# Kernel optimization log

Measured on AMD Instinct MI355X. Metric: run time of the kernel, lower is better.

The kernel has to match this reference:

```python
import math
import jax, jax.numpy as jnp
import numpy as np

B, L, D_MODEL, N_HEADS = 4, 4096, 1024, 16
HEAD_DIM = D_MODEL // N_HEADS
NUM_LANDMARKS = 128


def setup_inputs() -> dict:
    key = jax.random.key(0)
    ks = jax.random.split(key, 7)
    s = 1.0 / math.sqrt(D_MODEL)
    return {
        "x": jax.random.normal(ks[0], (B, L, D_MODEL), dtype=jnp.float32),
        "Wq": jax.random.uniform(ks[1], (D_MODEL, D_MODEL), jnp.float32, -s, s),
        "bq": jax.random.uniform(ks[2], (D_MODEL,), jnp.float32, -s, s),
        "Wk": jax.random.uniform(ks[3], (D_MODEL, D_MODEL), jnp.float32, -s, s),
        "bk": jax.random.uniform(ks[4], (D_MODEL,), jnp.float32, -s, s),
        "Wv": jax.random.uniform(ks[5], (D_MODEL, D_MODEL), jnp.float32, -s, s),
        "bv": jax.random.uniform(ks[6], (D_MODEL,), jnp.float32, -s, s),
    }


def _split_heads(t):
    b, l, _ = t.shape
    return t.reshape(b, l, N_HEADS, HEAD_DIM).transpose(0, 2, 1, 3)  # [b,h,l,d]


def _iterative_inv(mat, n_iter=6):
    # Newton-Schulz pseudo-inverse on [b,h,m,m]; 'original' init uses global max.
    I = jnp.eye(mat.shape[-1], dtype=mat.dtype)
    K = mat
    V = K.swapaxes(-1, -2) / jnp.max(jnp.sum(K, axis=-2))
    for _ in range(n_iter):
        KV = jnp.matmul(K, V)
        V = jnp.matmul(0.25 * V, 13.0 * I - jnp.matmul(KV, 15.0 * I - jnp.matmul(KV, 7.0 * I - KV)))
    return V


def reference(x, Wq, bq, Wk, bk, Wv, bv):
    Q = _split_heads(x @ Wq.T + bq)
    K = _split_heads(x @ Wk.T + bk)
    V = _split_heads(x @ Wv.T + bv)
    b, h, l, d = Q.shape
    # mask is internally all-ones (module overwrites any passed mask), so the
    # -1e9*(1-mask) bias term is identically zero and mask-multiplies are no-ops.
    scale = 1.0 / math.sqrt(math.sqrt(HEAD_DIM))
    Q = Q * scale
    K = K * scale
    seg = l // NUM_LANDMARKS
    Q_lm = Q.reshape(b, h, NUM_LANDMARKS, seg, d).mean(axis=-2)  # [b,h,m,d]
    K_lm = K.reshape(b, h, NUM_LANDMARKS, seg, d).mean(axis=-2)
    kernel_1 = jax.nn.softmax(jnp.einsum('bhld,bhmd->bhlm', Q, K_lm), axis=-1)   # [b,h,l,m]
    kernel_2 = jax.nn.softmax(jnp.einsum('bhmd,bhnd->bhmn', Q_lm, K_lm), axis=-1)  # [b,h,m,m]
    kernel_3 = jax.nn.softmax(jnp.einsum('bhmd,bhld->bhml', Q_lm, K), axis=-1)   # [b,h,m,l]
    X = jnp.matmul(jnp.matmul(kernel_1, _iterative_inv(kernel_2)), jnp.matmul(kernel_3, V))  # [b,h,l,d]
    out = X.transpose(0, 2, 1, 3).reshape(b, l, h * d)
    return out
```

## Files before the change

kernel.cpp:

```cpp
#include <hip/hip_runtime.h>
#include <hip/hip_bf16.h>
#include <stdint.h>

#define DEV __device__ __forceinline__

typedef __attribute__((ext_vector_type(8))) short bf16x8;
typedef __attribute__((ext_vector_type(4))) short short4v;
typedef __attribute__((ext_vector_type(4))) float f32x4;

static constexpr int LL = 4096;
static constexpr int NH = 16;
static constexpr int HD = 64;
static constexpr int DM = 1024;
static constexpr int NL = 128;
static constexpr int BH = 64;
static constexpr int NSPLIT = 8;
static constexpr float QK_SCALE = 0.35355339059327379f;

DEV short f2bf(float f) {
  union { __hip_bfloat16 h; short s; } u;
  u.h = __float2bfloat16(f);
  return u.s;
}
DEV float bf2f(unsigned short s) {
  union { unsigned u; float f; } u;
  u.u = ((unsigned)s) << 16;
  return u.f;
}
DEV float clampf(float v) {
  return fminf(fmaxf(v, -1e6f), 1e6f);
}

DEV f32x4 mfma16(bf16x8 a, bf16x8 b, f32x4 c) {
  return __builtin_amdgcn_mfma_f32_16x16x32_bf16(a, b, c, 0, 0, 0);
}

DEV void gl2lds16(const void* g, void* l) {
  __builtin_amdgcn_global_load_lds(
      (const __attribute__((address_space(1))) void*)g,
      (__attribute__((address_space(3))) void*)l, 16, 0, 0);
}

DEV void split1(float f, short& hi, short& lo) {
  unsigned u = __float_as_uint(f);
  hi = (short)(u >> 16);
  lo = f2bf(f - __uint_as_float(u & 0xffff0000u));
}

DEV void split8(const float* av, bf16x8& hv, bf16x8& lv) {
#pragma unroll
  for (int e = 0; e < 8; e++) {
    short hi, lo;
    split1(av[e], hi, lo);
    hv[e] = hi;
    lv[e] = lo;
  }
}

__global__ __launch_bounds__(256) void probe_kernel(
    const unsigned short* p0, const unsigned short* p1, const unsigned short* p2,
    const unsigned short* p3, const unsigned short* p4, const unsigned short* p5,
    const unsigned short* p6, int* flags)
{
  const unsigned short* ps[7] = {p0, p1, p2, p3, p4, p5, p6};
  const unsigned short* p = ps[blockIdx.x];
  const int t = threadIdx.x;
  __shared__ int cnt;
  if (t == 0) cnt = 0;
  __syncthreads();
  int c = 0;
  for (int i = t; i < 512; i += 256) {
    unsigned e = (p[2 * i] >> 7) & 0xFF;
    if (e > 90 && e < 160) c++;
  }
  atomicAdd(&cnt, c);
  __syncthreads();
  if (t == 0) flags[blockIdx.x] = (cnt < 358) ? 1 : 0;
}

__global__ __launch_bounds__(256) void cvtx_kernel(
    const void* __restrict__ src, const int* __restrict__ flags, int fidx,
    unsigned short* __restrict__ dst, int n8)
{
  const int f32 = flags[fidx];
  for (int i = blockIdx.x * 256 + threadIdx.x; i < n8; i += gridDim.x * 256) {
    if (f32) {
      const float* s = (const float*)src + (size_t)i * 8;
      f32x4 a = *(const f32x4*)s;
      f32x4 b = *(const f32x4*)(s + 4);
      bf16x8 o;
      o[0] = f2bf(a[0]); o[1] = f2bf(a[1]); o[2] = f2bf(a[2]); o[3] = f2bf(a[3]);
      o[4] = f2bf(b[0]); o[5] = f2bf(b[1]); o[6] = f2bf(b[2]); o[7] = f2bf(b[3]);
      *(bf16x8*)(dst + (size_t)i * 8) = o;
    } else {
      *(bf16x8*)(dst + (size_t)i * 8) =
          *(const bf16x8*)((const unsigned short*)src + (size_t)i * 8);
    }
  }
}

__global__ __launch_bounds__(256) void cvtw_kernel(
    const void* __restrict__ Wq, const void* __restrict__ Wk, const void* __restrict__ Wv,
    const void* __restrict__ bq, const void* __restrict__ bk, const void* __restrict__ bv,
    const int* __restrict__ flags,
    unsigned short* __restrict__ Wb, float* __restrict__ bb)
{
  const int bid = blockIdx.x, t = threadIdx.x;
  if (bid < 1536) {
    const int q = bid / 512;
    const int i = (bid % 512) * 256 + t;
    const void* src = (q == 0) ? Wq : ((q == 1) ? Wk : Wv);
    unsigned short* dst = Wb + (size_t)q * DM * DM;
    if (flags[1 + 2 * q]) {
      const float* s = (const float*)src + (size_t)i * 8;
      f32x4 a = *(const f32x4*)s;
      f32x4 b = *(const f32x4*)(s + 4);
      bf16x8 o;
      o[0] = f2bf(a[0]); o[1] = f2bf(a[1]); o[2] = f2bf(a[2]); o[3] = f2bf(a[3]);
      o[4] = f2bf(b[0]); o[5] = f2bf(b[1]); o[6] = f2bf(b[2]); o[7] = f2bf(b[3]);
      *(bf16x8*)(dst + (size_t)i * 8) = o;
    } else {
      *(bf16x8*)(dst + (size_t)i * 8) =
          *(const bf16x8*)((const unsigned short*)src + (size_t)i * 8);
    }
  } else {
    for (int i = t; i < 3 * DM; i += 256) {
      int q = i >> 10, idx = i & 1023;
      const void* src = (q == 0) ? bq : ((q == 1) ? bk : bv);
      bb[i] = flags[2 + 2 * q] ? ((const float*)src)[idx]
                               : bf2f(((const unsigned short*)src)[idx]);
    }
  }
}

__global__ __launch_bounds__(256, 2) void proj_kernel(
    const unsigned short* __restrict__ xb,
    const unsigned short* __restrict__ Wb,
    const float* __restrict__ bb,
    unsigned short* __restrict__ Qo, unsigned short* __restrict__ Ko,
    unsigned short* __restrict__ Vo,
    float* __restrict__ Qlm, float* __restrict__ Klm)
{
  __shared__ __align__(16) short As[2][128 * 32];
  __shared__ __align__(16) short Bs[2][128 * 32];

  const int t = threadIdx.x;
  const int w = t >> 6;
  const int l = t & 63;
  const int lane16 = l & 15, lgrp = l >> 4;

  const int bid = blockIdx.x;
  const int mt = bid & 127;
  const int nt = bid >> 7;
  const int which = nt >> 3;
  const int m0 = mt * 128;
  const int ncol0 = (nt & 7) * 128;

  unsigned short* outp = (which == 0) ? Qo : ((which == 1) ? Ko : Vo);
  const float scl = (which == 2) ? 1.0f : QK_SCALE;

  const int srow = w * 16 + (l >> 2);
  const int skc = (l & 3) * 8;
  const unsigned short* gA = xb + (size_t)(m0 + srow) * DM + skc;
  const unsigned short* gB = Wb + (size_t)which * DM * DM + (size_t)(ncol0 + srow) * DM + skc;
  short* lA0 = As[0] + w * 512;
  short* lA1 = As[1] + w * 512;
  short* lB0 = Bs[0] + w * 512;
  short* lB1 = Bs[1] + w * 512;

  const int wm = (w >> 1) * 64;
  const int wn = (w & 1) * 64;

  f32x4 acc[4][4];
#pragma unroll
  for (int i = 0; i < 4; i++)
#pragma unroll
    for (int j = 0; j < 4; j++) acc[i][j] = f32x4{0.f, 0.f, 0.f, 0.f};

  for (int kk = 0; kk < DM; kk += 64) {
    gl2lds16(gA + kk, lA0);
    gl2lds16(gA + kk + 64 * DM, lA0 + 2048);
    gl2lds16(gA + kk + 32, lA1);
    gl2lds16(gA + kk + 32 + 64 * DM, lA1 + 2048);
    gl2lds16(gB + kk, lB0);
    gl2lds16(gB + kk + 64 * DM, lB0 + 2048);
    gl2lds16(gB + kk + 32, lB1);
    gl2lds16(gB + kk + 32 + 64 * DM, lB1 + 2048);
    __syncthreads();
#pragma unroll
    for (int kc = 0; kc < 2; kc++) {
      bf16x8 af[4], bfv[4];
#pragma unroll
      for (int i = 0; i < 4; i++) {
        af[i]  = *(const bf16x8*)&As[kc][(wm + i * 16 + lane16) * 32 + lgrp * 8];
        bfv[i] = *(const bf16x8*)&Bs[kc][(wn + i * 16 + lane16) * 32 + lgrp * 8];
      }
#pragma unroll
      for (int i = 0; i < 4; i++)
#pragma unroll
        for (int j = 0; j < 4; j++)
          acc[i][j] = mfma16(af[i], bfv[j], acc[i][j]);
    }
    __syncthreads();
  }

  const int b = m0 >> 12;
  const int hh = (ncol0 + wn) >> 6;
  float bv4[4];
#pragma unroll
  for (int j = 0; j < 4; j++)
    bv4[j] = bb[which * DM + ncol0 + wn + j * 16 + lane16];

  float seg[2][4];
#pragma unroll
  for (int s = 0; s < 2; s++)
#pragma unroll
    for (int j = 0; j < 4; j++) seg[s][j] = 0.f;

#pragma unroll
  for (int i = 0; i < 4; i++) {
#pragma unroll
    for (int j = 0; j < 4; j++) {
#pragma unroll
      for (int r = 0; r < 4; r++) {
        float v = (acc[i][j][r] + bv4[j]) * scl;
        int row = wm + i * 16 + lgrp * 4 + r;
        int li = (m0 + row) & 4095;
        int dd = (wn + j * 16 + lane16) & 63;
        outp[(((size_t)(b * NH + hh)) * LL + li) * HD + dd] = (unsigned short)f2bf(v);
        seg[i >> 1][j] += v;
      }
    }
  }
  if (which < 2) {
    float* lmb = (which == 0) ? Qlm : Klm;
#pragma unroll
    for (int s = 0; s < 2; s++) {
#pragma unroll
      for (int j = 0; j < 4; j++) {
        float ssum = seg[s][j];
        ssum += __shfl_xor(ssum, 16, 64);
        ssum += __shfl_xor(ssum, 32, 64);
        if (lgrp == 0) {
          int m = ((m0 + wm + s * 32) & 4095) >> 5;
          int dd = (wn + j * 16 + lane16) & 63;
          lmb[(((size_t)(b * NH + hh)) * NL + m) * HD + dd] = clampf(ssum * (1.0f / 32.0f));
        }
      }
    }
  }
}

__global__ void lmcvt_kernel(const float* __restrict__ qf, const float* __restrict__ kf,
                             unsigned short* __restrict__ qb, unsigned short* __restrict__ kb)
{
  int i = blockIdx.x * 256 + threadIdx.x;
  if (i < BH * NL * HD) {
    qb[i] = (unsigned short)f2bf(qf[i]);
    kb[i] = (unsigned short)f2bf(kf[i]);
  }
}

__global__ __launch_bounds__(256, 1) void k2_kernel(
    const float* __restrict__ Qlm, const float* __restrict__ Klm,
    float* __restrict__ k2, float* __restrict__ colsum_g)
{
  __shared__ float cs[NL];
  const int bid = blockIdx.x;
  const int bh = bid >> 3;
  const int rc = bid & 7;
  const int t = threadIdx.x;
  const int r = t >> 4;
  const int c = t & 15;
  const int row = rc * 16 + r;
  const float* Q = Qlm + ((size_t)bh * NL + row) * HD;
  const float* K = Klm + (size_t)bh * NL * HD;
  float* k2p = k2 + (size_t)bh * NL * NL;

  for (int i = t; i < NL; i += 256) cs[i] = 0.f;

  f32x4 q4[16];
#pragma unroll
  for (int d = 0; d < 16; d++) q4[d] = *(const f32x4*)&Q[d * 4];

  float dots[8];
#pragma unroll
  for (int g = 0; g < 8; g++) {
    const float* kr = K + (size_t)(c + g * 16) * HD;
    float s = 0.f;
#pragma unroll
    for (int d = 0; d < 16; d++) {
      f32x4 k4 = *(const f32x4*)&kr[d * 4];
      s += q4[d][0] * k4[0];
      s += q4[d][1] * k4[1];
      s += q4[d][2] * k4[2];
      s += q4[d][3] * k4[3];
    }
    dots[g] = s;
  }

  float mx = dots[0];
#pragma unroll
  for (int g = 1; g < 8; g++) mx = fmaxf(mx, dots[g]);
  mx = fmaxf(mx, __shfl_xor(mx, 1, 16));
  mx = fmaxf(mx, __shfl_xor(mx, 2, 16));
  mx = fmaxf(mx, __shfl_xor(mx, 4, 16));
  mx = fmaxf(mx, __shfl_xor(mx, 8, 16));

  float sum = 0.f;
#pragma unroll
  for (int g = 0; g < 8; g++) {
    float e = __expf(dots[g] - mx);
    dots[g] = e;
    sum += e;
  }
  sum += __shfl_xor(sum, 1, 16);
  sum += __shfl_xor(sum, 2, 16);
  sum += __shfl_xor(sum, 4, 16);
  sum += __shfl_xor(sum, 8, 16);
  const float inv = 1.0f / fmaxf(sum, 1e-30f);

  __syncthreads();
#pragma unroll
  for (int g = 0; g < 8; g++) {
    float p = dots[g] * inv;
    k2p[(size_t)row * NL + c + g * 16] = p;
    atomicAdd(&cs[c + g * 16], p);
  }
  __syncthreads();
  for (int i = t; i < NL; i += 256) atomicAdd(&colsum_g[bh * NL + i], cs[i]);
}

__global__ __launch_bounds__(256) void alpha_kernel(
    const float* __restrict__ colsum_g, unsigned* __restrict__ alpha_bits)
{
  __shared__ float wm[4];
  const int t = threadIdx.x;
  float m = 0.f;
  for (int i = t; i < BH * NL; i += 256) m = fmaxf(m, colsum_g[i]);
#pragma unroll
  for (int o = 1; o < 64; o <<= 1) m = fmaxf(m, __shfl_xor(m, o, 64));
  if ((t & 63) == 0) wm[t >> 6] = m;
  __syncthreads();
  if (t == 0)
    *alpha_bits = __float_as_uint(fmaxf(fmaxf(wm[0], wm[1]), fmaxf(wm[2], wm[3])));
}

__global__ __launch_bounds__(256, 1) void k3v_kernel(
    const unsigned short* __restrict__ Qlmb, const unsigned short* __restrict__ K,
    const unsigned short* __restrict__ V,
    float* __restrict__ op, float* __restrict__ mp, float* __restrict__ lp)
{
  constexpr int LT = 64;
  constexpr int ST = 72;
  __shared__ __align__(16) short q_s[NL * ST];
  __shared__ __align__(16) short k_s[LT * ST];
  __shared__ __align__(16) short vt_s[HD * ST];
  __shared__ __align__(16) short p_s[NL * ST];

  const int bid = blockIdx.x;
  const int bh = bid >> 3;
  const int sp = bid & (NSPLIT - 1);
  const int t = threadIdx.x;
  const int w = t >> 6, l = t & 63;
  const int lane16 = l & 15, lgrp = l >> 4;
  const int wm = w * 32;
  const unsigned short* Kp = K + (size_t)bh * LL * HD;
  const unsigned short* Vp = V + (size_t)bh * LL * HD;

  for (int i = t; i < NL * HD / 4; i += 256) {
    int flat = i * 4, rr = flat >> 6, dd = flat & 63;
    *(uint2*)&q_s[rr * ST + dd] = *(const uint2*)&Qlmb[(size_t)bh * NL * HD + flat];
  }

  f32x4 oacc[2][4];
  float mrun[2][4], lrun[2][4];
#pragma unroll
  for (int i = 0; i < 2; i++)
#pragma unroll
    for (int j = 0; j < 4; j++) oacc[i][j] = f32x4{0.f, 0.f, 0.f, 0.f};
#pragma unroll
  for (int i = 0; i < 2; i++)
#pragma unroll
    for (int r = 0; r < 4; r++) { mrun[i][r] = -3.0e38f; lrun[i][r] = 0.f; }

  constexpr int TPS = LL / LT / NSPLIT;
  for (int lt = sp * TPS; lt < (sp + 1) * TPS; lt++) {
    const int l0 = lt * LT;
    for (int i = t; i < LT * HD / 4; i += 256) {
      int flat = i * 4, rr = flat >> 6, dd = flat & 63;
      *(uint2*)&k_s[rr * ST + dd] = *(const uint2*)&Kp[(size_t)(l0 + rr) * HD + dd];
      uint2 raw = *(const uint2*)&Vp[(size_t)(l0 + rr) * HD + dd];
      vt_s[(dd + 0) * ST + rr] = (short)(raw.x & 0xffff);
      vt_s[(dd + 1) * ST + rr] = (short)(raw.x >> 16);
      vt_s[(dd + 2) * ST + rr] = (short)(raw.y & 0xffff);
      vt_s[(dd + 3) * ST + rr] = (short)(raw.y >> 16);
    }
    __syncthreads();

    f32x4 sacc[2][4];
#pragma unroll
    for (int i = 0; i < 2; i++)
#pragma unroll
      for (int j = 0; j < 4; j++) sacc[i][j] = f32x4{0.f, 0.f, 0.f, 0.f};
#pragma unroll
    for (int kc = 0; kc < 2; kc++) {
      bf16x8 aq[2];
#pragma unroll
      for (int i = 0; i < 2; i++)
        aq[i] = *(const bf16x8*)&q_s[(wm + i * 16 + lane16) * ST + kc * 32 + lgrp * 8];
#pragma unroll
      for (int j = 0; j < 4; j++) {
        bf16x8 bk = *(const bf16x8*)&k_s[(j * 16 + lane16) * ST + kc * 32 + lgrp * 8];
#pragma unroll
        for (int i = 0; i < 2; i++) sacc[i][j] = mfma16(aq[i], bk, sacc[i][j]);
      }
    }

#pragma unroll
    for (int i = 0; i < 2; i++) {
#pragma unroll
      for (int r = 0; r < 4; r++) {
        float tm = fmaxf(fmaxf(sacc[i][0][r], sacc[i][1][r]),
                         fmaxf(sacc[i][2][r], sacc[i][3][r]));
        tm = fmaxf(tm, __shfl_xor(tm, 1, 16));
        tm = fmaxf(tm, __shfl_xor(tm, 2, 16));
        tm = fmaxf(tm, __shfl_xor(tm, 4, 16));
        tm = fmaxf(tm, __shfl_xor(tm, 8, 16));
        float mnew = fmaxf(mrun[i][r], tm);
        float al = __expf(mrun[i][r] - mnew);
        float rs = 0.f;
#pragma unroll
        for (int j = 0; j < 4; j++) {
          float e = __expf(sacc[i][j][r] - mnew);
          sacc[i][j][r] = e;
          rs += e;
        }
        rs += __shfl_xor(rs, 1, 16);
        rs += __shfl_xor(rs, 2, 16);
        rs += __shfl_xor(rs, 4, 16);
        rs += __shfl_xor(rs, 8, 16);
        lrun[i][r] = lrun[i][r] * al + rs;
        mrun[i][r] = mnew;
#pragma unroll
        for (int j = 0; j < 4; j++) oacc[i][j][r] *= al;
        int row = wm + i * 16 + lgrp * 4 + r;
#pragma unroll
        for (int j = 0; j < 4; j++)
          p_s[row * ST + j * 16 + lane16] = f2bf(sacc[i][j][r]);
      }
    }
    __syncthreads();

#pragma unroll
    for (int kc = 0; kc < 2; kc++) {
      bf16x8 ap[2];
#pragma unroll
      for (int i = 0; i < 2; i++)
        ap[i] = *(const bf16x8*)&p_s[(wm + i * 16 + lane16) * ST + kc * 32 + lgrp * 8];
#pragma unroll
      for (int j = 0; j < 4; j++) {
        bf16x8 bv = *(const bf16x8*)&vt_s[(j * 16 + lane16) * ST + kc * 32 + lgrp * 8];
#pragma unroll
        for (int i = 0; i < 2; i++) oacc[i][j] = mfma16(ap[i], bv, oacc[i][j]);
      }
    }
    __syncthreads();
  }

  float* opp = op + ((size_t)(bh * NSPLIT + sp)) * NL * HD;
#pragma unroll
  for (int i = 0; i < 2; i++)
#pragma unroll
    for (int j = 0; j < 4; j++)
#pragma unroll
      for (int r = 0; r < 4; r++) {
        int row = wm + i * 16 + lgrp * 4 + r;
        int dd = j * 16 + lane16;
        opp[(size_t)row * HD + dd] = oacc[i][j][r];
      }
  if (lane16 == 0) {
    const size_t base = (size_t)(bh * NSPLIT + sp) * NL;
#pragma unroll
    for (int i = 0; i < 2; i++)
#pragma unroll
      for (int r = 0; r < 4; r++) {
        int row = wm + i * 16 + lgrp * 4 + r;
        mp[base + row] = mrun[i][r];
        lp[base + row] = lrun[i][r];
      }
  }
}

__global__ __launch_bounds__(256) void k3v_combine(
    const float* __restrict__ op, const float* __restrict__ mp,
    const float* __restrict__ lp, float* __restrict__ k3v)
{
  const int idx = blockIdx.x * 256 + threadIdx.x;
  const int dd = idx & 63;
  const int row = (idx >> 6) & 127;
  const int bh = idx >> 13;
  (void)dd;
  float m = -3.0e38f;
  float ms[NSPLIT];
#pragma unroll
  for (int s = 0; s < NSPLIT; s++) {
    ms[s] = mp[(size_t)(bh * NSPLIT + s) * NL + row];
    m = fmaxf(m, ms[s]);
  }
  float o = 0.f, ltot = 0.f;
#pragma unroll
  for (int s = 0; s < NSPLIT; s++) {
    float sc = __expf(ms[s] - m);
    ltot += lp[(size_t)(bh * NSPLIT + s) * NL + row] * sc;
    o += op[((size_t)(bh * NSPLIT + s) * NL + row) * HD + dd] * sc;
  }
  k3v[idx] = clampf(o / fmaxf(ltot, 1e-30f));
}

__global__ __launch_bounds__(512, 1) void ns_kernel(
    const float* __restrict__ k2, const unsigned* __restrict__ alpha_bits,
    const float* __restrict__ k3v, unsigned short* __restrict__ w2t)
{
  constexpr int VST = 132;
  constexpr int BST = 136;
  __shared__ __align__(16) float Vf[NL * VST];
  __shared__ __align__(16) short Bth[NL * BST];
  __shared__ __align__(16) short Btl[NL * BST];

  const int bh = blockIdx.x, t = threadIdx.x;
  const int w = t >> 6, l = t & 63;
  const int lane16 = l & 15, lgrp = l >> 4;
  const float* K2 = k2 + (size_t)bh * NL * NL;

  bf16x8 k2hi[4], k2lo[4];
#pragma unroll
  for (int kk = 0; kk < 4; kk++) {
    const float* ap = K2 + (size_t)(w * 16 + lane16) * NL + kk * 32 + lgrp * 8;
    f32x4 a0 = *(const f32x4*)ap;
    f32x4 a1 = *(const f32x4*)(ap + 4);
    float av[8] = {a0[0], a0[1], a0[2], a0[3], a1[0], a1[1], a1[2], a1[3]};
    split8(av, k2hi[kk], k2lo[kk]);
  }

  const float inva = 1.0f / fmaxf(__uint_as_float(*alpha_bits), 1e-30f);
  for (int i = t; i < NL * NL; i += 512) {
    int rr = i >> 7, cc = i & 127;
    float v = clampf(K2[(size_t)cc * NL + rr] * inva);
    Vf[rr * VST + cc] = v;
    short hi, lo; split1(v, hi, lo);
    Bth[cc * BST + rr] = hi;
    Btl[cc * BST + rr] = lo;
  }
  __syncthreads();

  f32x4 macc[8], vacc[8];

  auto mmA = [&](const bf16x8* ahi, const bf16x8* alo) {
#pragma unroll
    for (int j = 0; j < 8; j++) macc[j] = f32x4{0.f, 0.f, 0.f, 0.f};
#pragma unroll
    for (int kk = 0; kk < 4; kk++) {
#pragma unroll
      for (int j = 0; j < 8; j++) {
        const int bo = (j * 16 + lane16) * BST + kk * 32 + lgrp * 8;
        bf16x8 bh_ = *(const bf16x8*)&Bth[bo];
        bf16x8 bl_ = *(const bf16x8*)&Btl[bo];
        macc[j] = mfma16(alo[kk], bh_, macc[j]);
        macc[j] = mfma16(ahi[kk], bl_, macc[j]);
        macc[j] = mfma16(ahi[kk], bh_, macc[j]);
      }
    }
  };

  auto mmV = [&]() {
    bf16x8 ahi[4], alo[4];
#pragma unroll
    for (int kk = 0; kk < 4; kk++) {
      const float* ap = &Vf[(w * 16 + lane16) * VST + kk * 32 + lgrp * 8];
      f32x4 a0 = *(const f32x4*)ap;
      f32x4 a1 = *(const f32x4*)(ap + 4);
      float av[8] = {a0[0], a0[1], a0[2], a0[3], a1[0], a1[1], a1[2], a1[3]};
      split8(av, ahi[kk], alo[kk]);
    }
    mmA(ahi, alo);
  };

  auto writeBt = [&]() {
#pragma unroll
    for (int j = 0; j < 8; j++) {
      short4v hv, lv;
#pragma unroll
      for (int r = 0; r < 4; r++) {
        float c = clampf(macc[j][r]);
        short hi, lo; split1(c, hi, lo);
        hv[r] = hi; lv[r] = lo;
      }
      const int base = (j * 16 + lane16) * BST + w * 16 + lgrp * 4;
      *(short4v*)&Bth[base] = hv;
      *(short4v*)&Btl[base] = lv;
    }
  };

  for (int it = 0; it < 6; it++) {
    mmA(k2hi, k2lo);
    __syncthreads();
    writeBt();
    __syncthreads();

    mmV();
#pragma unroll
    for (int j = 0; j < 8; j++)
#pragma unroll
      for (int r = 0; r < 4; r++)
        vacc[j][r] = 3.25f * Vf[(w * 16 + lgrp * 4 + r) * VST + j * 16 + lane16]
                   - 3.75f * macc[j][r];
    __syncthreads();
#pragma unroll
    for (int j = 0; j < 8; j++)
#pragma unroll
      for (int r = 0; r < 4; r++)
        Vf[(w * 16 + lgrp * 4 + r) * VST + j * 16 + lane16] = clampf(macc[j][r]);
    __syncthreads();

    mmV();
#pragma unroll
    for (int j = 0; j < 8; j++)
#pragma unroll
      for (int r = 0; r < 4; r++) vacc[j][r] += 1.75f * macc[j][r];
    __syncthreads();
#pragma unroll
    for (int j = 0; j < 8; j++)
#pragma unroll
      for (int r = 0; r < 4; r++)
        Vf[(w * 16 + lgrp * 4 + r) * VST + j * 16 + lane16] = clampf(macc[j][r]);
    __syncthreads();

    mmV();
    __syncthreads();
#pragma unroll
    for (int j = 0; j < 8; j++) {
      short4v hv, lv;
#pragma unroll
      for (int r = 0; r < 4; r++) {
        float v = clampf(vacc[j][r] - 0.25f * macc[j][r]);
        Vf[(w * 16 + lgrp * 4 + r) * VST + j * 16 + lane16] = v;
        short hi, lo; split1(v, hi, lo);
        hv[r] = hi; lv[r] = lo;
      }
      const int base = (j * 16 + lane16) * BST + w * 16 + lgrp * 4;
      *(short4v*)&Bth[base] = hv;
      *(short4v*)&Btl[base] = lv;
    }
    __syncthreads();
  }

  const float* kvp = k3v + (size_t)bh * NL * HD;
  for (int i = t; i < NL * HD; i += 512) {
    int rr = i >> 6, dd = i & 63;
    float f = kvp[i];
    short hi, lo; split1(f, hi, lo);
    Bth[dd * BST + rr] = hi;
    Btl[dd * BST + rr] = lo;
  }
  __syncthreads();

  const int wr = (w & 3);
  const int wc = (w >> 2);
  f32x4 oacc[4];
#pragma unroll
  for (int j = 0; j < 4; j++) oacc[j] = f32x4{0.f, 0.f, 0.f, 0.f};
#pragma unroll
  for (int kk = 0; kk < 4; kk++) {
    const int ao = (wr * 16 + lane16) * BST + kk * 32 + lgrp * 8;
    bf16x8 ahi = *(const bf16x8*)&Bth[ao];
    bf16x8 alo = *(const bf16x8*)&Btl[ao];
#pragma unroll
    for (int j = 0; j < 4; j++) {
      const float* bp = &Vf[((wc * 4 + j) * 16 + lane16) * VST + kk * 32 + lgrp * 8];
      f32x4 b0 = *(const f32x4*)bp;
      f32x4 b1 = *(const f32x4*)(bp + 4);
      float bvv[8] = {b0[0], b0[1], b0[2], b0[3], b1[0], b1[1], b1[2], b1[3]};
      bf16x8 bhv, blv;
      split8(bvv, bhv, blv);
      oacc[j] = mfma16(alo, bhv, oacc[j]);
      oacc[j] = mfma16(ahi, blv, oacc[j]);
      oacc[j] = mfma16(ahi, bhv, oacc[j]);
    }
  }
  unsigned short* outp = w2t + (size_t)bh * HD * NL;
#pragma unroll
  for (int j = 0; j < 4; j++)
#pragma unroll
    for (int r = 0; r < 4; r++) {
      int dd = wr * 16 + lgrp * 4 + r;
      int m  = (wc * 4 + j) * 16 + lane16;
      outp[(size_t)dd * NL + m] = (unsigned short)f2bf(clampf(oacc[j][r]));
    }
}

__global__ __launch_bounds__(256, 2) void final_kernel(
    const unsigned short* __restrict__ Q, const unsigned short* __restrict__ Klmb,
    const unsigned short* __restrict__ w2t, float* __restrict__ outp)
{
  constexpr int KSD = 72;
  constexpr int PSD = 136;
  __shared__ __align__(16) short klm_s[NL * KSD];
  __shared__ __align__(16) short p_s[NL * PSD];

  const int bid = blockIdx.x;
  const int bh = bid >> 5, lt = bid & 31;
  const int l0 = lt * NL;
  const int t = threadIdx.x, w = t >> 6, l = t & 63;
  const int lane16 = l & 15, lgrp = l >> 4;
  const int wm = w * 32;
  const unsigned short* Qp = Q + (size_t)bh * LL * HD;
  const unsigned short* Kp = Klmb + (size_t)bh * NL * HD;
  const unsigned short* Wp = w2t + (size_t)bh * HD * NL;

  for (int i = t; i < NL * HD / 4; i += 256) {
    int flat = i * 4, rr = flat >> 6, dd = flat & 63;
    *(uint2*)&klm_s[rr * KSD + dd] = *(const uint2*)&Kp[flat];
  }
  __syncthreads();

  f32x4 sacc[2][8];
#pragma unroll
  for (int i = 0; i < 2; i++)
#pragma unroll
    for (int j = 0; j < 8; j++) sacc[i][j] = f32x4{0.f, 0.f, 0.f, 0.f};
#pragma unroll
  for (int kc = 0; kc < 2; kc++) {
    bf16x8 aq[2];
#pragma unroll
    for (int i = 0; i < 2; i++)
      aq[i] = *(const bf16x8*)&Qp[(size_t)(l0 + wm + i * 16 + lane16) * HD + kc * 32 + lgrp * 8];
#pragma unroll
    for (int j = 0; j < 8; j++) {
      bf16x8 bk = *(const bf16x8*)&klm_s[(j * 16 + lane16) * KSD + kc * 32 + lgrp * 8];
#pragma unroll
      for (int i = 0; i < 2; i++) sacc[i][j] = mfma16(aq[i], bk, sacc[i][j]);
    }
  }

#pragma unroll
  for (int i = 0; i < 2; i++) {
#pragma unroll
    for (int r = 0; r < 4; r++) {
      float mx = -1e30f;
#pragma unroll
      for (int j = 0; j < 8; j++) mx = fmaxf(mx, sacc[i][j][r]);
      mx = fmaxf(mx, __shfl_xor(mx, 1, 16));
      mx = fmaxf(mx, __shfl_xor(mx, 2, 16));
      mx = fmaxf(mx, __shfl_xor(mx, 4, 16));
      mx = fmaxf(mx, __shfl_xor(mx, 8, 16));
      float sum = 0.f;
#pragma unroll
      for (int j = 0; j < 8; j++) {
        float e = __expf(sacc[i][j][r] - mx);
        sacc[i][j][r] = e;
        sum += e;
      }
      sum += __shfl_xor(sum, 1, 16);
      sum += __shfl_xor(sum, 2, 16);
      sum += __shfl_xor(sum, 4, 16);
      sum += __shfl_xor(sum, 8, 16);
      float inv = 1.0f / fmaxf(sum, 1e-30f);
      int row = wm + i * 16 + lgrp * 4 + r;
#pragma unroll
      for (int j = 0; j < 8; j++)
        p_s[row * PSD + j * 16 + lane16] = f2bf(sacc[i][j][r] * inv);
    }
  }
  __syncthreads();

  f32x4 oacc[2][4];
#pragma unroll
  for (int i = 0; i < 2; i++)
#pragma unroll
    for (int j = 0; j < 4; j++) oacc[i][j] = f32x4{0.f, 0.f, 0.f, 0.f};
#pragma unroll
  for (int kc = 0; kc < 4; kc++) {
    bf16x8 ap[2];
#pragma unroll
    for (int i = 0; i < 2; i++)
      ap[i] = *(const bf16x8*)&p_s[(wm + i * 16 + lane16) * PSD + kc * 32 + lgrp * 8];
#pragma unroll
    for (int j = 0; j < 4; j++) {
      bf16x8 bw = *(const bf16x8*)&Wp[(size_t)(j * 16 + lane16) * NL + kc * 32 + lgrp * 8];
#pragma unroll
      for (int i = 0; i < 2; i++) oacc[i][j] = mfma16(ap[i], bw, oacc[i][j]);
    }
  }

  const int b = bh >> 4, h = bh & 15;
#pragma unroll
  for (int i = 0; i < 2; i++)
#pragma unroll
    for (int j = 0; j < 4; j++)
#pragma unroll
      for (int r = 0; r < 4; r++) {
        int row = wm + i * 16 + lgrp * 4 + r;
        int dd = j * 16 + lane16;
        outp[((size_t)b * LL + l0 + row) * DM + h * HD + dd] = oacc[i][j][r];
      }
}

extern "C" void kernel_launch(void* const* d_in, const int* in_sizes, int n_in,
                              void* d_out, int out_size, void* d_ws, size_t ws_size,
                              hipStream_t stream) {
  (void)in_sizes; (void)n_in; (void)out_size; (void)ws_size;
  float* outp = (float*)d_out;

  char* ws = (char*)d_ws;
  size_t off = 0;
  auto alloc = [&](size_t bytes) -> void* {
    void* p = ws + off;
    off += (bytes + 255) & ~(size_t)255;
    return p;
  };
  int* flags = (int*)alloc(64);
  unsigned* alpha_bits = (unsigned*)alloc(64);
  float* colsum_g = (float*)alloc((size_t)BH * NL * 4);
  float* Qlm = (float*)alloc((size_t)BH * NL * HD * 4);
  float* Klm = (float*)alloc((size_t)BH * NL * HD * 4);
  unsigned short* Qlmb = (unsigned short*)alloc((size_t)BH * NL * HD * 2);
  unsigned short* Klmb = (unsigned short*)alloc((size_t)BH * NL * HD * 2);
  float* k2 = (float*)alloc((size_t)BH * NL * NL * 4);
  float* k3v = (float*)alloc((size_t)BH * NL * HD * 4);
  unsigned short* w2t = (unsigned short*)alloc((size_t)BH * HD * NL * 2);
  unsigned short* Wb = (unsigned short*)alloc((size_t)3 * DM * DM * 2);
  float* bb = (float*)alloc((size_t)3 * DM * 4);
  const size_t XB_BYTES = (size_t)4 * LL * DM * 2;
  char* ub = (char*)alloc(XB_BYTES);
  unsigned short* xb = (unsigned short*)ub;
  float* op = (float*)ub;
  float* mp = (float*)(ub + (size_t)BH * NSPLIT * NL * HD * 4);
  float* lp = mp + (size_t)BH * NSPLIT * NL;
  const size_t QKV = (size_t)BH * LL * HD;
  unsigned short* Qb = (unsigned short*)alloc(QKV * 2);
  unsigned short* Kb = (unsigned short*)alloc(QKV * 2);
  unsigned short* Vb = (unsigned short*)alloc(QKV * 2);

  hipMemsetAsync(colsum_g, 0, (size_t)BH * NL * 4, stream);
  probe_kernel<<<7, 256, 0, stream>>>(
      (const unsigned short*)d_in[0], (const unsigned short*)d_in[1],
      (const unsigned short*)d_in[2], (const unsigned short*)d_in[3],
      (const unsigned short*)d_in[4], (const unsigned short*)d_in[5],
      (const unsigned short*)d_in[6], flags);
  cvtx_kernel<<<2048, 256, 0, stream>>>(d_in[0], flags, 0, xb, 4 * LL * DM / 8);
  cvtw_kernel<<<1537, 256, 0, stream>>>(
      d_in[1], d_in[3], d_in[5], d_in[2], d_in[4], d_in[6], flags, Wb, bb);
  proj_kernel<<<128 * 24, 256, 0, stream>>>(xb, Wb, bb, Qb, Kb, Vb, Qlm, Klm);
  lmcvt_kernel<<<(BH * NL * HD + 255) / 256, 256, 0, stream>>>(Qlm, Klm, Qlmb, Klmb);
  k2_kernel<<<BH * 8, 256, 0, stream>>>(Qlm, Klm, k2, colsum_g);
  alpha_kernel<<<1, 256, 0, stream>>>(colsum_g, alpha_bits);
  k3v_kernel<<<BH * NSPLIT, 256, 0, stream>>>(Qlmb, Kb, Vb, op, mp, lp);
  k3v_combine<<<BH * NL * HD / 256, 256, 0, stream>>>(op, mp, lp, k3v);
  ns_kernel<<<BH, 512, 0, stream>>>(k2, alpha_bits, k3v, w2t);
  final_kernel<<<BH * 32, 256, 0, stream>>>(Qb, Klmb, w2t, outp);
}
```

Measured before the change: 471.7 us.

## Fuse landmark bf16 conversion and split-softmax combine; double k3v split count

The bf16 landmark copies are now written directly in the projection epilogue, which removes the separate lmcvt kernel. The split-K combine for kernel_3·V is folded into the Newton-Schulz kernel's load of k3v, which removes the k3v_combine launch and its intermediate buffer. NSPLIT goes from 8 to 16 so that k3v_kernel launches 1024 blocks and fills the GPU better. In exchange, ns_kernel's serial preamble must read 16 partials per element, and partial buffer traffic grows.

```diff
diff --git a/kernel.cpp b/kernel.cpp
--- a/kernel.cpp
+++ b/kernel.cpp
@@ -14,7 +14,7 @@
 static constexpr int DM = 1024;
 static constexpr int NL = 128;
 static constexpr int BH = 64;
-static constexpr int NSPLIT = 8;
+static constexpr int NSPLIT = 16;
 static constexpr float QK_SCALE = 0.35355339059327379f;
 
 DEV short f2bf(float f) {
@@ -139,7 +139,8 @@
     const float* __restrict__ bb,
     unsigned short* __restrict__ Qo, unsigned short* __restrict__ Ko,
     unsigned short* __restrict__ Vo,
-    float* __restrict__ Qlm, float* __restrict__ Klm)
+    float* __restrict__ Qlm, float* __restrict__ Klm,
+    unsigned short* __restrict__ Qlmb, unsigned short* __restrict__ Klmb)
 {
   __shared__ __align__(16) short As[2][128 * 32];
   __shared__ __align__(16) short Bs[2][128 * 32];
@@ -234,6 +235,7 @@
   }
   if (which < 2) {
     float* lmb = (which == 0) ? Qlm : Klm;
+    unsigned short* lmbb = (which == 0) ? Qlmb : Klmb;
 #pragma unroll
     for (int s = 0; s < 2; s++) {
 #pragma unroll
@@ -244,20 +246,13 @@
         if (lgrp == 0) {
           int m = ((m0 + wm + s * 32) & 4095) >> 5;
           int dd = (wn + j * 16 + lane16) & 63;
-          lmb[(((size_t)(b * NH + hh)) * NL + m) * HD + dd] = clampf(ssum * (1.0f / 32.0f));
+          float mv = clampf(ssum * (1.0f / 32.0f));
+          size_t idx = (((size_t)(b * NH + hh)) * NL + m) * HD + dd;
+          lmb[idx] = mv;
+          lmbb[idx] = (unsigned short)f2bf(mv);
         }
       }
     }
-  }
-}
-
-__global__ void lmcvt_kernel(const float* __restrict__ qf, const float* __restrict__ kf,
-                             unsigned short* __restrict__ qb, unsigned short* __restrict__ kb)
-{
-  int i = blockIdx.x * 256 + threadIdx.x;
-  if (i < BH * NL * HD) {
-    qb[i] = (unsigned short)f2bf(qf[i]);
-    kb[i] = (unsigned short)f2bf(kf[i]);
   }
 }
 
@@ -359,7 +354,7 @@
   __shared__ __align__(16) short p_s[NL * ST];
 
   const int bid = blockIdx.x;
-  const int bh = bid >> 3;
+  const int bh = bid >> 4;
   const int sp = bid & (NSPLIT - 1);
   const int t = threadIdx.x;
   const int w = t >> 6, l = t & 63;
@@ -492,35 +487,10 @@
   }
 }
 
-__global__ __launch_bounds__(256) void k3v_combine(
-    const float* __restrict__ op, const float* __restrict__ mp,
-    const float* __restrict__ lp, float* __restrict__ k3v)
-{
-  const int idx = blockIdx.x * 256 + threadIdx.x;
-  const int dd = idx & 63;
-  const int row = (idx >> 6) & 127;
-  const int bh = idx >> 13;
-  (void)dd;
-  float m = -3.0e38f;
-  float ms[NSPLIT];
-#pragma unroll
-  for (int s = 0; s < NSPLIT; s++) {
-    ms[s] = mp[(size_t)(bh * NSPLIT + s) * NL + row];
-    m = fmaxf(m, ms[s]);
-  }
-  float o = 0.f, ltot = 0.f;
-#pragma unroll
-  for (int s = 0; s < NSPLIT; s++) {
-    float sc = __expf(ms[s] - m);
-    ltot += lp[(size_t)(bh * NSPLIT + s) * NL + row] * sc;
-    o += op[((size_t)(bh * NSPLIT + s) * NL + row) * HD + dd] * sc;
-  }
-  k3v[idx] = clampf(o / fmaxf(ltot, 1e-30f));
-}
-
 __global__ __launch_bounds__(512, 1) void ns_kernel(
     const float* __restrict__ k2, const unsigned* __restrict__ alpha_bits,
-    const float* __restrict__ k3v, unsigned short* __restrict__ w2t)
+    const float* __restrict__ op, const float* __restrict__ mp,
+    const float* __restrict__ lp, unsigned short* __restrict__ w2t)
 {
   constexpr int VST = 132;
   constexpr int BST = 136;
@@ -655,10 +625,26 @@
     __syncthreads();
   }
 
-  const float* kvp = k3v + (size_t)bh * NL * HD;
+  const float* opp = op + (size_t)bh * NSPLIT * NL * HD;
+  const float* mpp = mp + (size_t)bh * NSPLIT * NL;
+  const float* lpp = lp + (size_t)bh * NSPLIT * NL;
   for (int i = t; i < NL * HD; i += 512) {
     int rr = i >> 6, dd = i & 63;
-    float f = kvp[i];
+    float ms[NSPLIT];
+    float m = -3.0e38f;
+#pragma unroll
+    for (int s = 0; s < NSPLIT; s++) {
+      ms[s] = mpp[(size_t)s * NL + rr];
+      m = fmaxf(m, ms[s]);
+    }
+    float o = 0.f, lt_ = 0.f;
+#pragma unroll
+    for (int s = 0; s < NSPLIT; s++) {
+      float sc = __expf(ms[s] - m);
+      lt_ += lpp[(size_t)s * NL + rr] * sc;
+      o += opp[((size_t)s * NL + rr) * HD + dd] * sc;
+    }
+    float f = clampf(o / fmaxf(lt_, 1e-30f));
     short hi, lo; split1(f, hi, lo);
     Bth[dd * BST + rr] = hi;
     Btl[dd * BST + rr] = lo;
@@ -827,15 +813,17 @@
   unsigned short* Qlmb = (unsigned short*)alloc((size_t)BH * NL * HD * 2);
   unsigned short* Klmb = (unsigned short*)alloc((size_t)BH * NL * HD * 2);
   float* k2 = (float*)alloc((size_t)BH * NL * NL * 4);
-  float* k3v = (float*)alloc((size_t)BH * NL * HD * 4);
   unsigned short* w2t = (unsigned short*)alloc((size_t)BH * HD * NL * 2);
   unsigned short* Wb = (unsigned short*)alloc((size_t)3 * DM * DM * 2);
   float* bb = (float*)alloc((size_t)3 * DM * 4);
+  const size_t OP_BYTES = (size_t)BH * NSPLIT * NL * HD * 4;
+  const size_t ML_BYTES = (size_t)BH * NSPLIT * NL * 4;
   const size_t XB_BYTES = (size_t)4 * LL * DM * 2;
-  char* ub = (char*)alloc(XB_BYTES);
+  const size_t UB_BYTES = OP_BYTES + 2 * ML_BYTES + 512;
+  char* ub = (char*)alloc(UB_BYTES > XB_BYTES ? UB_BYTES : XB_BYTES);
   unsigned short* xb = (unsigned short*)ub;
   float* op = (float*)ub;
-  float* mp = (float*)(ub + (size_t)BH * NSPLIT * NL * HD * 4);
+  float* mp = (float*)(ub + OP_BYTES);
   float* lp = mp + (size_t)BH * NSPLIT * NL;
   const size_t QKV = (size_t)BH * LL * HD;
   unsigned short* Qb = (unsigned short*)alloc(QKV * 2);
@@ -851,12 +839,11 @@
   cvtx_kernel<<<2048, 256, 0, stream>>>(d_in[0], flags, 0, xb, 4 * LL * DM / 8);
   cvtw_kernel<<<1537, 256, 0, stream>>>(
       d_in[1], d_in[3], d_in[5], d_in[2], d_in[4], d_in[6], flags, Wb, bb);
-  proj_kernel<<<128 * 24, 256, 0, stream>>>(xb, Wb, bb, Qb, Kb, Vb, Qlm, Klm);
-  lmcvt_kernel<<<(BH * NL * HD + 255) / 256, 256, 0, stream>>>(Qlm, Klm, Qlmb, Klmb);
+  proj_kernel<<<128 * 24, 256, 0, stream>>>(xb, Wb, bb, Qb, Kb, Vb,
+                                            Qlm, Klm, Qlmb, Klmb);
   k2_kernel<<<BH * 8, 256, 0, stream>>>(Qlm, Klm, k2, colsum_g);
   alpha_kernel<<<1, 256, 0, stream>>>(colsum_g, alpha_bits);
   k3v_kernel<<<BH * NSPLIT, 256, 0, stream>>>(Qlmb, Kb, Vb, op, mp, lp);
-  k3v_combine<<<BH * NL * HD / 256, 256, 0, stream>>>(op, mp, lp, k3v);
-  ns_kernel<<<BH, 512, 0, stream>>>(k2, alpha_bits, k3v, w2t);
+  ns_kernel<<<BH, 512, 0, stream>>>(k2, alpha_bits, op, mp, lp, w2t);
   final_kernel<<<BH * 32, 256, 0, stream>>>(Qb, Klmb, w2t, outp);
 }
```

New measurement: 481.2 us. 1.02x slower.
